# Kernel tuning notes

Measured on AMD Instinct MI355X. Metric: run time of the kernel, lower is better.

Reference implementation:

```python
import jax, jax.numpy as jnp
import numpy as np

THR = 1.0                      # spike threshold
DECAY_V = float(np.exp(-1.0 / 20.0))
GAMMA = 0.3                    # surrogate-gradient dampening factor
OUT_DECAY = 0.8                # exp_convolve decay

@jax.custom_vjp
def spike_fn(v_scaled):
    # Heaviside spike with pseudo-derivative gamma*max(0, 1-|v_scaled|)
    return (v_scaled > 0.0).astype(v_scaled.dtype)

def _spike_fwd(v_scaled):
    return spike_fn(v_scaled), v_scaled

def _spike_bwd(v_scaled, g):
    return (g * GAMMA * jnp.maximum(0.0, 1.0 - jnp.abs(v_scaled)),)

spike_fn.defvjp(_spike_fwd, _spike_bwd)


def setup_inputs() -> dict:
    key = jax.random.key(0)
    k1, k2, k3, k4 = jax.random.split(key, 4)
    B, T, NI, NR = 32, 1000, 128, 512
    inputs = jax.random.normal(k1, (B, T, NI), dtype=jnp.float32)
    w_in = jax.random.normal(k2, (NI, NR), dtype=jnp.float32) / np.sqrt(NI)
    w_rec = jax.random.normal(k3, (NR, NR), dtype=jnp.float32) / np.sqrt(NR)
    w_out = jax.random.normal(k4, (NR, 1), dtype=jnp.float32) / np.sqrt(NR)
    b_out = jnp.zeros((1,), dtype=jnp.float32)
    return {"inputs": inputs, "w_in": w_in, "w_rec": w_rec, "w_out": w_out, "b_out": b_out}


def reference(inputs, w_in, w_rec, w_out, b_out):
    B, T, _ = inputs.shape
    NR = w_rec.shape[0]
    dtype = inputs.dtype
    # no autapses (zero diagonal on recurrent weights, as in LSNN cells)
    w_rec_masked = w_rec * (1.0 - jnp.eye(NR, dtype=dtype))
    # precompute feedforward input currents: [T, B, NR]
    i_in = jnp.swapaxes(jnp.einsum('bti,iu->btu', inputs, w_in), 0, 1)

    def lif_step(carry, x_t):
        v, z = carry
        i_t = x_t + z @ w_rec_masked           # [B, NR]
        v_new = DECAY_V * v + i_t - z * THR    # reset by subtraction
        z_new = spike_fn((v_new - THR) / THR)
        return (v_new, z_new), (v_new, z_new)

    v0 = jnp.zeros((B, NR), dtype)
    z0 = jnp.zeros((B, NR), dtype)
    _, (vs, zs) = jax.lax.scan(lif_step, (v0, z0), i_in)
    voltages = jnp.swapaxes(vs, 0, 1)  # [B, T, NR]
    spikes = jnp.swapaxes(zs, 0, 1)    # [B, T, NR]

    proj = spikes @ w_out + b_out      # [B, T, 1]

    def filt_step(a, x):
        a_new = OUT_DECAY * a + (1.0 - OUT_DECAY) * x
        return a_new, a_new

    f0 = jnp.zeros((B, 1), dtype)
    _, pred = jax.lax.scan(filt_step, f0, jnp.swapaxes(proj, 0, 1))
    prediction = jnp.swapaxes(pred, 0, 1)  # [B, T, 1]
    return voltages, spikes, prediction
```

## Files before the change

kernel.cpp:

```cpp
#include <hip/hip_runtime.h>

#define NR 512
#define NI 128
#define B 32
#define T 1000
#define G 32

__device__ __forceinline__ float mul_nofma(float a, float b) {
    float r = a * b;
    asm volatile("" : "+v"(r));
    return r;
}

__device__ __forceinline__ void bar_lds() {
    asm volatile("s_waitcnt lgkmcnt(0)\n\ts_barrier" ::: "memory");
}

__global__ __launch_bounds__(512) void k_prep(const float* __restrict__ w_rec,
                                              float* __restrict__ w_ws) {
    const int r = blockIdx.x, u = threadIdx.x;
    float val = 0.f;
    if (r < NR && r != u) val = w_rec[r * NR + u];
    w_ws[r * NR + u] = val;
}

template <int ROWS>
__global__ __launch_bounds__(512) void k_in_gemm(const float* __restrict__ inputs,
                                                 const float* __restrict__ w_in,
                                                 float* __restrict__ i_in) {
    const int u = threadIdx.x;
    const int r0 = blockIdx.x * ROWS;
    float acc[ROWS];
#pragma unroll
    for (int r = 0; r < ROWS; ++r) acc[r] = 0.f;
    const float* __restrict__ inp = inputs + (long)r0 * NI;
#pragma unroll 4
    for (int i = 0; i < NI; ++i) {
        float w = w_in[i * NR + u];
#pragma unroll
        for (int r = 0; r < ROWS; ++r)
            acc[r] = __builtin_fmaf(inp[r * NI + i], w, acc[r]);
    }
#pragma unroll
    for (int r = 0; r < ROWS; ++r)
        i_in[(long)(r0 + r) * NR + u] = acc[r];
}

__device__ __forceinline__ void loadg1(float (&buf)[G], const int* __restrict__ lp,
                                       const float* __restrict__ w_ws, int u) {
#pragma unroll
    for (int qq = 0; qq < G / 4; ++qq) {
        int4 jv = *(const int4*)(lp + qq * 4);
        const float* r0 = w_ws + (__builtin_amdgcn_readfirstlane(jv.x) << 9);
        const float* r1 = w_ws + (__builtin_amdgcn_readfirstlane(jv.y) << 9);
        const float* r2 = w_ws + (__builtin_amdgcn_readfirstlane(jv.z) << 9);
        const float* r3 = w_ws + (__builtin_amdgcn_readfirstlane(jv.w) << 9);
        buf[qq * 4 + 0] = r0[u];
        buf[qq * 4 + 1] = r1[u];
        buf[qq * 4 + 2] = r2[u];
        buf[qq * 4 + 3] = r3[u];
    }
}

__device__ __forceinline__ void sumg1(const float (&buf)[G], float& s) {
#pragma unroll
    for (int q = 0; q < G; ++q) s = __fadd_rn(s, buf[q]);
}

__global__ __launch_bounds__(1024) void k_scan(const float* __restrict__ w_ws,
                                               float* __restrict__ out) {
    const int b = blockIdx.x;
    const int tid = threadIdx.x;
    const int u = tid & (NR - 1);
    const int h = tid >> 9;
    const int wav = tid >> 6;
    const int lane = tid & 63;

    float* __restrict__ volt_b = out + (long)b * (T * NR);
    float* __restrict__ spk_b  = out + (long)B * T * NR + (long)b * (T * NR);

    __shared__ __align__(16) int listA[256];
    __shared__ __align__(16) int listB[256];
    __shared__ int wcnt[8];
    __shared__ float shs[2][NR];

    float v = 0.f, z = 0.f;
    const float decay = 0.951229424500714f;
    __syncthreads();

    for (int t = 0; t < T; ++t) {
        float ii = volt_b[t * NR + u];

        unsigned long long m = __ballot(z > 0.5f);
        if (h == 0 && lane == 0) wcnt[wav] = __popcll(m);
        bar_lds();

        const int c0 = wcnt[0], c1 = wcnt[1], c2 = wcnt[2], c3 = wcnt[3];
        const int c4 = wcnt[4], c5 = wcnt[5], c6 = wcnt[6], c7 = wcnt[7];
        const int cnt_lo = c0 + c1 + c2 + c3;
        const int cnt_hi = c4 + c5 + c6 + c7;

        if (h == 0) {
            if (z > 0.5f) {
                int below = __popcll(m & ((1ull << lane) - 1ull));
                if (wav < 4) {
                    int pos = (wav > 0 ? c0 : 0) + (wav > 1 ? c1 : 0) + (wav > 2 ? c2 : 0) + below;
                    listA[pos] = u;
                } else {
                    int pos = (wav > 4 ? c4 : 0) + (wav > 5 ? c5 : 0) + (wav > 6 ? c6 : 0) + below;
                    listB[pos] = u;
                }
            }
            if (u < 256) { if (u >= cnt_lo) listA[u] = NR; }
            else         { int x = u - 256; if (x >= cnt_hi) listB[x] = NR; }
        }
        bar_lds();

        const int* lp  = h ? listB : listA;
        const int  myn = h ? ((cnt_hi + G - 1) / G) : ((cnt_lo + G - 1) / G);
        float s = 0.f;
        if (myn > 0) {
            float bA[G], bB[G];
            loadg1(bA, lp, w_ws, u);
            int g = 0;
            while (true) {
                if (g + 1 < myn) loadg1(bB, lp + (g + 1) * G, w_ws, u);
                sumg1(bA, s);
                ++g;
                if (g == myn) break;
                if (g + 1 < myn) loadg1(bA, lp + (g + 1) * G, w_ws, u);
                sumg1(bB, s);
                ++g;
                if (g == myn) break;
            }
        }
        shs[h][u] = s;
        bar_lds();

        float rec = __fadd_rn(shs[0][u], shs[1][u]);
        float it = __fadd_rn(ii, rec);
        float m1 = mul_nofma(decay, v);
        float t2 = __fadd_rn(m1, it);
        float vn = __fsub_rn(t2, z);
        float zn = (vn > 1.0f) ? 1.0f : 0.0f;
        if (h == 0) {
            volt_b[t * NR + u] = vn;
            spk_b[t * NR + u]  = zn;
        }
        v = vn; z = zn;
    }
}

__global__ __launch_bounds__(512) void k_pred(const float* __restrict__ w_out,
                                              const float* __restrict__ b_out,
                                              float* __restrict__ out) {
    const int b = blockIdx.x;
    const int tid = threadIdx.x;
    const int wav = tid >> 6, lane = tid & 63;
    const float* __restrict__ spk_b = out + (long)B * T * NR + (long)b * (T * NR);
    float* __restrict__ pred = out + 2L * B * T * NR + (long)b * T;

    __shared__ double projs[T];

    double wo[8];
#pragma unroll
    for (int q = 0; q < 8; ++q) wo[q] = (double)w_out[lane + q * 64];

    for (int t = wav; t < T; t += 8) {
        double p = 0.0;
#pragma unroll
        for (int q = 0; q < 8; ++q)
            p += (double)spk_b[t * NR + lane + q * 64] * wo[q];
#pragma unroll
        for (int o = 32; o > 0; o >>= 1) p += __shfl_xor(p, o, 64);
        if (lane == 0) projs[t] = p;
    }
    __syncthreads();
    if (tid == 0) {
        const double bo = (double)b_out[0];
        double ema = 0.0;
        for (int t = 0; t < T; ++t) {
            ema = 0.8 * ema + 0.2 * (bo + projs[t]);
            pred[t] = (float)ema;
        }
    }
}

__global__ __launch_bounds__(512) void k_scan_ref(const float* __restrict__ w_rec,
                                                  const float* __restrict__ w_out,
                                                  const float* __restrict__ b_out,
                                                  float* __restrict__ out) {
    const int b = blockIdx.x;
    const int u = threadIdx.x;
    const int wav = u >> 6, lane = u & 63;
    const int KC = 256;

    float* __restrict__ volt_b = out + (long)b * (T * NR);
    float* __restrict__ spk_b  = out + (long)B * T * NR + (long)b * (T * NR);
    float* __restrict__ pred   = out + 2L * B * T * NR;

    __shared__ __align__(16) int list[NR];
    __shared__ int wcnt[8];
    __shared__ double projp[8];

    float v = 0.f, z = 0.f;
    const float decay = 0.951229424500714f;
    const double wo = (double)w_out[u];
    const double bo = (double)b_out[0];
    double ema = 0.0;

    for (int t = 0; t < T; ++t) {
        unsigned long long m = __ballot(z > 0.5f);
        if (lane == 0) wcnt[wav] = __popcll(m);
        __syncthreads();
        int cnt = 0, base = 0;
#pragma unroll
        for (int w2 = 0; w2 < 8; ++w2) {
            int c = wcnt[w2];
            if (w2 < wav) base += c;
            cnt += c;
        }
        if (z > 0.5f) {
            int pos = base + __popcll(m & ((1ull << lane) - 1ull));
            list[pos] = u;
        }
        float ii = volt_b[t * NR + u];
        __syncthreads();

        float s1 = 0.f, s2 = 0.f;
        int k = 0;
        for (; k + 8 <= cnt; k += 8) {
            int4 ja = *(const int4*)&list[k];
            int4 jb = *(const int4*)&list[k + 4];
            int j0 = __builtin_amdgcn_readfirstlane(ja.x);
            int j1 = __builtin_amdgcn_readfirstlane(ja.y);
            int j2 = __builtin_amdgcn_readfirstlane(ja.z);
            int j3 = __builtin_amdgcn_readfirstlane(ja.w);
            int j4 = __builtin_amdgcn_readfirstlane(jb.x);
            int j5 = __builtin_amdgcn_readfirstlane(jb.y);
            int j6 = __builtin_amdgcn_readfirstlane(jb.z);
            int j7 = __builtin_amdgcn_readfirstlane(jb.w);
            float w0 = w_rec[j0 * NR + u]; if (j0 == u) w0 = 0.f;
            float w1 = w_rec[j1 * NR + u]; if (j1 == u) w1 = 0.f;
            float w2 = w_rec[j2 * NR + u]; if (j2 == u) w2 = 0.f;
            float w3 = w_rec[j3 * NR + u]; if (j3 == u) w3 = 0.f;
            float w4 = w_rec[j4 * NR + u]; if (j4 == u) w4 = 0.f;
            float w5 = w_rec[j5 * NR + u]; if (j5 == u) w5 = 0.f;
            float w6 = w_rec[j6 * NR + u]; if (j6 == u) w6 = 0.f;
            float w7 = w_rec[j7 * NR + u]; if (j7 == u) w7 = 0.f;
            if (j0 < KC) s1 = __fadd_rn(s1, w0); else s2 = __fadd_rn(s2, w0);
            if (j1 < KC) s1 = __fadd_rn(s1, w1); else s2 = __fadd_rn(s2, w1);
            if (j2 < KC) s1 = __fadd_rn(s1, w2); else s2 = __fadd_rn(s2, w2);
            if (j3 < KC) s1 = __fadd_rn(s1, w3); else s2 = __fadd_rn(s2, w3);
            if (j4 < KC) s1 = __fadd_rn(s1, w4); else s2 = __fadd_rn(s2, w4);
            if (j5 < KC) s1 = __fadd_rn(s1, w5); else s2 = __fadd_rn(s2, w5);
            if (j6 < KC) s1 = __fadd_rn(s1, w6); else s2 = __fadd_rn(s2, w6);
            if (j7 < KC) s1 = __fadd_rn(s1, w7); else s2 = __fadd_rn(s2, w7);
        }
        for (; k < cnt; ++k) {
            int j = __builtin_amdgcn_readfirstlane(list[k]);
            float w = w_rec[j * NR + u];
            if (j == u) w = 0.f;
            if (j < KC) s1 = __fadd_rn(s1, w); else s2 = __fadd_rn(s2, w);
        }
        float rec = __fadd_rn(s1, s2);

        float it = __fadd_rn(ii, rec);
        float m1 = mul_nofma(decay, v);
        float t2 = __fadd_rn(m1, it);
        float vn = __fsub_rn(t2, z);
        float zn = (vn > 1.0f) ? 1.0f : 0.0f;
        volt_b[t * NR + u] = vn;
        spk_b[t * NR + u]  = zn;

        double p = (double)zn * wo;
#pragma unroll
        for (int o = 32; o > 0; o >>= 1) p += __shfl_xor(p, o, 64);
        if (lane == 0) projp[wav] = p;
        __syncthreads();
        if (u == 0) {
            double pr = bo;
#pragma unroll
            for (int w2 = 0; w2 < 8; ++w2) pr += projp[w2];
            ema = 0.8 * ema + 0.2 * pr;
            pred[b * T + t] = (float)ema;
        }
        v = vn; z = zn;
    }
}

extern "C" void kernel_launch(void* const* d_in, const int* in_sizes, int n_in,
                              void* d_out, int out_size, void* d_ws, size_t ws_size,
                              hipStream_t stream) {
    const float* inputs = (const float*)d_in[0];
    const float* w_in   = (const float*)d_in[1];
    const float* w_rec  = (const float*)d_in[2];
    const float* w_out  = (const float*)d_in[3];
    const float* b_out  = (const float*)d_in[4];
    float* out = (float*)d_out;

    k_in_gemm<16><<<dim3(B * T / 16), dim3(512), 0, stream>>>(inputs, w_in, out);

    const size_t need = (size_t)(NR + 1) * NR * sizeof(float);
    if (ws_size >= need) {
        float* w_ws = (float*)d_ws;
        k_prep<<<dim3(NR + 1), dim3(512), 0, stream>>>(w_rec, w_ws);
        k_scan<<<dim3(B), dim3(1024), 0, stream>>>(w_ws, out);
        k_pred<<<dim3(B), dim3(512), 0, stream>>>(w_out, b_out, out);
    } else {
        k_scan_ref<<<dim3(B), dim3(512), 0, stream>>>(w_rec, w_out, b_out, out);
    }
}
```

Measured before the change: 2.216 ms.

## Halve scan block size, each thread gathers two adjacent columns with float2 loads

The recurrent scan kernel drops from 1024 to 512 threads per batch block. Each half of the block still handles one half of the spike list, but every thread now loads two adjacent weight columns per spiking row as a float2 and keeps two accumulators. The group size falls from 32 to 16 so the register footprint stays similar. This halves the thread count and the barrier participants per timestep and widens each memory access, at the cost of less latency hiding per block and more serial add work per thread.

```diff
diff --git a/kernel.cpp b/kernel.cpp
--- a/kernel.cpp
+++ b/kernel.cpp
@@ -4,7 +4,8 @@
 #define NI 128
 #define B 32
 #define T 1000
-#define G 32
+#define G2 16
+typedef float v2f __attribute__((ext_vector_type(2)));
 
 __device__ __forceinline__ float mul_nofma(float a, float b) {
     float r = a * b;
@@ -46,35 +47,38 @@
         i_in[(long)(r0 + r) * NR + u] = acc[r];
 }
 
-__device__ __forceinline__ void loadg1(float (&buf)[G], const int* __restrict__ lp,
-                                       const float* __restrict__ w_ws, int u) {
-#pragma unroll
-    for (int qq = 0; qq < G / 4; ++qq) {
+__device__ __forceinline__ void loadg2(v2f (&buf)[G2], const int* __restrict__ lp,
+                                       const float* __restrict__ w_ws, int c2) {
+#pragma unroll
+    for (int qq = 0; qq < G2 / 4; ++qq) {
         int4 jv = *(const int4*)(lp + qq * 4);
         const float* r0 = w_ws + (__builtin_amdgcn_readfirstlane(jv.x) << 9);
         const float* r1 = w_ws + (__builtin_amdgcn_readfirstlane(jv.y) << 9);
         const float* r2 = w_ws + (__builtin_amdgcn_readfirstlane(jv.z) << 9);
         const float* r3 = w_ws + (__builtin_amdgcn_readfirstlane(jv.w) << 9);
-        buf[qq * 4 + 0] = r0[u];
-        buf[qq * 4 + 1] = r1[u];
-        buf[qq * 4 + 2] = r2[u];
-        buf[qq * 4 + 3] = r3[u];
-    }
-}
-
-__device__ __forceinline__ void sumg1(const float (&buf)[G], float& s) {
-#pragma unroll
-    for (int q = 0; q < G; ++q) s = __fadd_rn(s, buf[q]);
-}
-
-__global__ __launch_bounds__(1024) void k_scan(const float* __restrict__ w_ws,
-                                               float* __restrict__ out) {
+        buf[qq * 4 + 0] = *(const v2f*)&r0[c2];
+        buf[qq * 4 + 1] = *(const v2f*)&r1[c2];
+        buf[qq * 4 + 2] = *(const v2f*)&r2[c2];
+        buf[qq * 4 + 3] = *(const v2f*)&r3[c2];
+    }
+}
+
+__device__ __forceinline__ void sumg2(const v2f (&buf)[G2], float& sx, float& sy) {
+#pragma unroll
+    for (int q = 0; q < G2; ++q) {
+        sx = __fadd_rn(sx, buf[q].x);
+        sy = __fadd_rn(sy, buf[q].y);
+    }
+}
+
+__global__ __launch_bounds__(512) void k_scan(const float* __restrict__ w_ws,
+                                              float* __restrict__ out) {
     const int b = blockIdx.x;
     const int tid = threadIdx.x;
-    const int u = tid & (NR - 1);
-    const int h = tid >> 9;
-    const int wav = tid >> 6;
-    const int lane = tid & 63;
+    const int u = tid;
+    const int wav = tid >> 6, lane = tid & 63;
+    const int h = tid >> 8;
+    const int c2 = (tid & 255) << 1;
 
     float* __restrict__ volt_b = out + (long)b * (T * NR);
     float* __restrict__ spk_b  = out + (long)B * T * NR + (long)b * (T * NR);
@@ -82,7 +86,7 @@
     __shared__ __align__(16) int listA[256];
     __shared__ __align__(16) int listB[256];
     __shared__ int wcnt[8];
-    __shared__ float shs[2][NR];
+    __shared__ __align__(16) float shs[2][NR];
 
     float v = 0.f, z = 0.f;
     const float decay = 0.951229424500714f;
@@ -92,49 +96,48 @@
         float ii = volt_b[t * NR + u];
 
         unsigned long long m = __ballot(z > 0.5f);
-        if (h == 0 && lane == 0) wcnt[wav] = __popcll(m);
+        if (lane == 0) wcnt[wav] = __popcll(m);
         bar_lds();
 
-        const int c0 = wcnt[0], c1 = wcnt[1], c2 = wcnt[2], c3 = wcnt[3];
+        const int c0 = wcnt[0], c1 = wcnt[1], cc2 = wcnt[2], c3 = wcnt[3];
         const int c4 = wcnt[4], c5 = wcnt[5], c6 = wcnt[6], c7 = wcnt[7];
-        const int cnt_lo = c0 + c1 + c2 + c3;
+        const int cnt_lo = c0 + c1 + cc2 + c3;
         const int cnt_hi = c4 + c5 + c6 + c7;
 
-        if (h == 0) {
-            if (z > 0.5f) {
-                int below = __popcll(m & ((1ull << lane) - 1ull));
-                if (wav < 4) {
-                    int pos = (wav > 0 ? c0 : 0) + (wav > 1 ? c1 : 0) + (wav > 2 ? c2 : 0) + below;
-                    listA[pos] = u;
-                } else {
-                    int pos = (wav > 4 ? c4 : 0) + (wav > 5 ? c5 : 0) + (wav > 6 ? c6 : 0) + below;
-                    listB[pos] = u;
-                }
+        if (z > 0.5f) {
+            int below = __popcll(m & ((1ull << lane) - 1ull));
+            if (wav < 4) {
+                int pos = (wav > 0 ? c0 : 0) + (wav > 1 ? c1 : 0) + (wav > 2 ? cc2 : 0) + below;
+                listA[pos] = u;
+            } else {
+                int pos = (wav > 4 ? c4 : 0) + (wav > 5 ? c5 : 0) + (wav > 6 ? c6 : 0) + below;
+                listB[pos] = u;
             }
-            if (u < 256) { if (u >= cnt_lo) listA[u] = NR; }
-            else         { int x = u - 256; if (x >= cnt_hi) listB[x] = NR; }
-        }
+        }
+        if (u < 256) { if (u >= cnt_lo) listA[u] = NR; }
+        else         { int x = u - 256; if (x >= cnt_hi) listB[x] = NR; }
         bar_lds();
 
         const int* lp  = h ? listB : listA;
-        const int  myn = h ? ((cnt_hi + G - 1) / G) : ((cnt_lo + G - 1) / G);
-        float s = 0.f;
+        const int  cnt = h ? cnt_hi : cnt_lo;
+        const int  myn = (cnt + G2 - 1) / G2;
+        float sx = 0.f, sy = 0.f;
         if (myn > 0) {
-            float bA[G], bB[G];
-            loadg1(bA, lp, w_ws, u);
+            v2f bA[G2], bB[G2];
+            loadg2(bA, lp, w_ws, c2);
             int g = 0;
             while (true) {
-                if (g + 1 < myn) loadg1(bB, lp + (g + 1) * G, w_ws, u);
-                sumg1(bA, s);
+                if (g + 1 < myn) loadg2(bB, lp + (g + 1) * G2, w_ws, c2);
+                sumg2(bA, sx, sy);
                 ++g;
                 if (g == myn) break;
-                if (g + 1 < myn) loadg1(bA, lp + (g + 1) * G, w_ws, u);
-                sumg1(bB, s);
+                if (g + 1 < myn) loadg2(bA, lp + (g + 1) * G2, w_ws, c2);
+                sumg2(bB, sx, sy);
                 ++g;
                 if (g == myn) break;
             }
         }
-        shs[h][u] = s;
+        *(v2f*)&shs[h][c2] = (v2f){sx, sy};
         bar_lds();
 
         float rec = __fadd_rn(shs[0][u], shs[1][u]);
@@ -143,10 +146,8 @@
         float t2 = __fadd_rn(m1, it);
         float vn = __fsub_rn(t2, z);
         float zn = (vn > 1.0f) ? 1.0f : 0.0f;
-        if (h == 0) {
-            volt_b[t * NR + u] = vn;
-            spk_b[t * NR + u]  = zn;
-        }
+        volt_b[t * NR + u] = vn;
+        spk_b[t * NR + u]  = zn;
         v = vn; z = zn;
     }
 }
@@ -305,7 +306,7 @@
     if (ws_size >= need) {
         float* w_ws = (float*)d_ws;
         k_prep<<<dim3(NR + 1), dim3(512), 0, stream>>>(w_rec, w_ws);
-        k_scan<<<dim3(B), dim3(1024), 0, stream>>>(w_ws, out);
+        k_scan<<<dim3(B), dim3(512), 0, stream>>>(w_ws, out);
         k_pred<<<dim3(B), dim3(512), 0, stream>>>(w_out, b_out, out);
     } else {
         k_scan_ref<<<dim3(B), dim3(512), 0, stream>>>(w_rec, w_out, b_out, out);
```

Result: slower. 2.814 ms (+27.0%).
